# Kernel optimization log

Measured on AMD Instinct MI355X. Metric: run time of the kernel, lower is better.

Reference implementation:

```python
import jax, jax.numpy as jnp
import numpy as np

N_NODES = 100000
N_EDGES = 1600000
DIM = 64
BN_EPS = 1e-5


def setup_inputs() -> dict:
    key = jax.random.key(0)
    ks = jax.random.split(key, 6)
    x = jax.random.normal(ks[0], (N_NODES, DIM), dtype=jnp.float32)
    edge_index = jax.random.randint(ks[1], (2, N_EDGES), 0, N_NODES, dtype=jnp.int32)
    W = jax.random.normal(ks[2], (DIM, DIM), dtype=jnp.float32) / np.sqrt(DIM)
    b = jax.random.normal(ks[3], (DIM,), dtype=jnp.float32) * 0.01
    gamma = jnp.ones((DIM,), dtype=jnp.float32)
    beta = jnp.zeros((DIM,), dtype=jnp.float32)
    return {"x": x, "edge_index": edge_index, "W": W, "b": b, "gamma": gamma, "beta": beta}


def reference(x, edge_index, W, b, gamma, beta):
    n = x.shape[0]
    src, dst = edge_index[0], edge_index[1]
    # GCNConv adds self loops
    loop = jnp.arange(n, dtype=edge_index.dtype)
    src = jnp.concatenate([src, loop])
    dst = jnp.concatenate([dst, loop])
    # symmetric degree normalization: D^-1/2 (A+I) D^-1/2
    deg = jax.ops.segment_sum(jnp.ones(src.shape[0], x.dtype), dst, num_segments=n)
    dinv = jnp.where(deg > 0, jax.lax.rsqrt(deg), 0.0)
    norm = dinv[src] * dinv[dst]  # [E+N]
    h = x @ W  # [N, D] transform before aggregation (GCN order)
    msg = h[src] * norm[:, None]  # gather + scale
    out = jax.ops.segment_sum(msg, dst, num_segments=n) + b  # scatter-add
    # BatchNorm1d (training mode: batch statistics, biased variance)
    mean = jnp.mean(out, axis=0)
    var = jnp.mean(jnp.square(out - mean), axis=0)
    out = (out - mean) * jax.lax.rsqrt(var + BN_EPS) * gamma + beta
    # ReLU; dropout is identity in eval mode
    return jax.nn.relu(out)
```

## Files before the change

### kernel.cpp

```cpp
#include <hip/hip_runtime.h>

#define N_NODES 100000
#define N_EDGES 1600000
#define DIM 64
#define BN_EPS 1e-5f

#define BNODES 128
#define NBUCK ((N_NODES + BNODES - 1) / BNODES)
#define CAP_RAW 2560
#define CAP_OUT 3584
#define TILE 4096
#define ABLK ((N_EDGES + TILE - 1) / TILE)

#define GBLK 6250

typedef __bf16 bf16x8 __attribute__((ext_vector_type(8)));
typedef float floatx4 __attribute__((ext_vector_type(4)));

static __device__ __forceinline__ unsigned short f2bf(float f) {
    unsigned u = __float_as_uint(f);
    u = (u + 0x7FFFu + ((u >> 16) & 1u)) >> 16;
    return (unsigned short)u;
}
static __device__ __forceinline__ float bf2f(unsigned short h) {
    return __uint_as_float(((unsigned)h) << 16);
}

__global__ void __launch_bounds__(1024)
passA_kernel(const int* __restrict__ src, const int* __restrict__ dst,
             int* __restrict__ cur, unsigned int* __restrict__ entries, int E) {
    __shared__ int hist[NBUCK];
    __shared__ int lbase[NBUCK];
    int t = threadIdx.x;
    if (t < NBUCK) hist[t] = 0;
    __syncthreads();

    int e0   = blockIdx.x * TILE;
    int eend = min(e0 + TILE, E);

    int dreg[4], sreg[4], ne = 0;
    for (int e = e0 + t; e < eend; e += 1024) {
        dreg[ne] = dst[e];
        sreg[ne] = src[e];
        atomicAdd(&hist[dreg[ne] >> 7], 1);
        ++ne;
    }
    __syncthreads();
    if (t < NBUCK) {
        int ii = t + (blockIdx.x * 331) % NBUCK;
        if (ii >= NBUCK) ii -= NBUCK;
        int c = hist[ii];
        lbase[ii] = (c > 0) ? atomicAdd(&cur[ii], c) : 0;
        hist[ii] = 0;
    }
    __syncthreads();
    for (int k = 0; k < ne; ++k) {
        int s = sreg[k];
        int d = dreg[k];
        int b = d >> 7;
        int r = atomicAdd(&hist[b], 1);
        int pos = lbase[b] + r;
        if (pos < CAP_RAW)
            entries[(size_t)b * CAP_OUT + pos] = ((unsigned)s << 7) | (unsigned)(d & 127);
    }
}

__global__ void __launch_bounds__(256)
build_kernel(unsigned int* __restrict__ entries, const int* __restrict__ cur,
             int* __restrict__ rowbeg, int* __restrict__ rowend,
             float* __restrict__ dinv,
             const float* __restrict__ x, const float* __restrict__ W,
             unsigned short* __restrict__ hb, int dummyIdx, int N) {
    __shared__ unsigned int raw[CAP_RAW];
    __shared__ int hist[BNODES];
    __shared__ int sbuf[BNODES];
    __shared__ int startx[BNODES];
    __shared__ int cursor[BNODES];
    __shared__ float sdinv[BNODES];
    int bucket = blockIdx.x;
    int t = threadIdx.x;
    int node0 = bucket * BNODES;
    int nn = min(BNODES, N - node0);
    int cnt = min(cur[bucket], CAP_RAW);
    unsigned int* eb = entries + (size_t)bucket * CAP_OUT;

    if (t < BNODES) hist[t] = 0;
    __syncthreads();
    for (int i = t; i < cnt; i += 256) {
        unsigned int e = eb[i];
        raw[i] = e;
        atomicAdd(&hist[e & 127], 1);
    }
    __syncthreads();
    int pdeg_t = 0;
    if (t < BNODES) { pdeg_t = (hist[t] + 7) & ~7; sbuf[t] = pdeg_t; }
    __syncthreads();
    for (int off = 1; off < BNODES; off <<= 1) {
        int add = (t < BNODES && t >= off) ? sbuf[t - off] : 0;
        __syncthreads();
        if (t < BNODES) sbuf[t] += add;
        __syncthreads();
    }
    if (t < BNODES) {
        int ex = sbuf[t] - pdeg_t;
        startx[t] = ex;
        cursor[t] = ex;
    }
    __syncthreads();
    for (int i = t; i < cnt; i += 256) {
        unsigned int e = raw[i];
        int d = e & 127;
        int p = atomicAdd(&cursor[d], 1);
        eb[p] = e >> 7;
    }
    if (t < nn) {
        int dg  = hist[t];
        int pdg = (dg + 7) & ~7;
        int base = startx[t];
        for (int k = dg; k < pdg; ++k) eb[base + k] = (unsigned)dummyIdx;
        int gbase = bucket * CAP_OUT + base;
        rowbeg[node0 + t] = gbase;
        rowend[node0 + t] = gbase + pdg;
        float di = rsqrtf((float)(dg + 1));
        dinv[node0 + t] = di;
        sdinv[t] = di;
    }
    __syncthreads();

    int lane = t & 63, wv = t >> 6;
    int m = lane & 15, quad = lane >> 4;
    int nchunk = nn >> 4;
    if (wv < nchunk || nchunk == 8) {
        bf16x8 bfrag[2][4];
#pragma unroll
        for (int c = 0; c < 2; ++c)
#pragma unroll
            for (int nt = 0; nt < 4; ++nt) {
                bf16x8 f;
#pragma unroll
                for (int j = 0; j < 8; ++j) {
                    int k = c * 32 + quad * 8 + j;
                    f[j] = (__bf16)W[k * DIM + nt * 16 + m];
                }
                bfrag[c][nt] = f;
            }
        for (int c2 = wv; c2 < nchunk; c2 += 4) {
            int lrow0 = c2 * 16;
            int row0 = node0 + lrow0;
            const float* xr = x + (size_t)(row0 + m) * DIM;
            bf16x8 afrag[2];
#pragma unroll
            for (int c = 0; c < 2; ++c) {
                float4 lo = *(const float4*)(xr + c * 32 + quad * 8);
                float4 hi = *(const float4*)(xr + c * 32 + quad * 8 + 4);
                bf16x8 f;
                f[0] = (__bf16)lo.x; f[1] = (__bf16)lo.y; f[2] = (__bf16)lo.z; f[3] = (__bf16)lo.w;
                f[4] = (__bf16)hi.x; f[5] = (__bf16)hi.y; f[6] = (__bf16)hi.z; f[7] = (__bf16)hi.w;
                afrag[c] = f;
            }
            float dv[4];
#pragma unroll
            for (int r = 0; r < 4; ++r) dv[r] = sdinv[lrow0 + quad * 4 + r];
#pragma unroll
            for (int nt = 0; nt < 4; ++nt) {
                floatx4 acc = {0.f, 0.f, 0.f, 0.f};
                acc = __builtin_amdgcn_mfma_f32_16x16x32_bf16(afrag[0], bfrag[0][nt], acc, 0, 0, 0);
                acc = __builtin_amdgcn_mfma_f32_16x16x32_bf16(afrag[1], bfrag[1][nt], acc, 0, 0, 0);
#pragma unroll
                for (int r = 0; r < 4; ++r) {
                    int row = row0 + quad * 4 + r;
                    hb[(size_t)row * DIM + nt * 16 + m] = f2bf(acc[r] * dv[r]);
                }
            }
        }
    }
}

__global__ void __launch_bounds__(256)
gather_kernel(const int* __restrict__ rowbeg, const int* __restrict__ rowend,
              const unsigned int* __restrict__ srt, const unsigned short* __restrict__ hb,
              const float* __restrict__ dinv, float* __restrict__ out,
              float* __restrict__ partial, int N) {
    __shared__ float red[2][4][64];
    int lane = threadIdx.x & 63;
    int wv   = threadIdx.x >> 6;
    int g    = blockIdx.x * 4 + wv;
    int n0   = g << 2;
    float s_sum = 0.f, s_sq = 0.f;

    if (n0 < N) {
        int beg = __builtin_amdgcn_readfirstlane(rowbeg[n0]);
        int s1  = __builtin_amdgcn_readfirstlane(rowbeg[n0 + 1]);
        int s2  = __builtin_amdgcn_readfirstlane(rowbeg[n0 + 2]);
        int s3  = __builtin_amdgcn_readfirstlane(rowbeg[n0 + 3]);
        int end = __builtin_amdgcn_readfirstlane(rowend[n0 + 3]);
        float acc0 = 0.f, acc1 = 0.f, acc2 = 0.f, acc3 = 0.f;

        for (int base = beg; base < end; base += 64) {
            int idx = base + lane;
            unsigned int sv = (idx < end) ? srt[idx] : 0u;
            int cn = min(64, end - base);
            for (int j = 0; j < cn; j += 8) {
                int p0 = base + j;
                int k = (p0 >= s1) + (p0 >= s2) + (p0 >= s3);
                float v[8];
#pragma unroll
                for (int u = 0; u < 8; ++u) {
                    unsigned int s = (unsigned)__shfl((int)sv, j + u, 64);
                    v[u] = bf2f(hb[(size_t)s * DIM + lane]);
                }
                float csum = ((v[0] + v[1]) + (v[2] + v[3])) +
                             ((v[4] + v[5]) + (v[6] + v[7]));
                acc0 += (k == 0) ? csum : 0.f;
                acc1 += (k == 1) ? csum : 0.f;
                acc2 += (k == 2) ? csum : 0.f;
                acc3 += (k == 3) ? csum : 0.f;
            }
        }

        float v0 = (acc0 + bf2f(hb[(size_t)(n0 + 0) * DIM + lane])) * dinv[n0 + 0];
        float v1 = (acc1 + bf2f(hb[(size_t)(n0 + 1) * DIM + lane])) * dinv[n0 + 1];
        float v2 = (acc2 + bf2f(hb[(size_t)(n0 + 2) * DIM + lane])) * dinv[n0 + 2];
        float v3 = (acc3 + bf2f(hb[(size_t)(n0 + 3) * DIM + lane])) * dinv[n0 + 3];
        out[(size_t)(n0 + 0) * DIM + lane] = v0;
        out[(size_t)(n0 + 1) * DIM + lane] = v1;
        out[(size_t)(n0 + 2) * DIM + lane] = v2;
        out[(size_t)(n0 + 3) * DIM + lane] = v3;
        s_sum = ((v0 + v1) + (v2 + v3));
        s_sq  = ((v0 * v0 + v1 * v1) + (v2 * v2 + v3 * v3));
    }

    red[0][wv][lane] = s_sum;
    red[1][wv][lane] = s_sq;
    __syncthreads();
    if (threadIdx.x < 64) {
        int c = threadIdx.x;
        partial[(size_t)blockIdx.x * 128 + c] =
            red[0][0][c] + red[0][1][c] + red[0][2][c] + red[0][3][c];
        partial[(size_t)blockIdx.x * 128 + 64 + c] =
            red[1][0][c] + red[1][1][c] + red[1][2][c] + red[1][3][c];
    }
}

__global__ void reduce2_kernel(const float* __restrict__ partial, float* __restrict__ gstat) {
    __shared__ float buf[256];
    int t = threadIdx.x;
    int col = t & 127;
    int half = t >> 7;
    int r0 = blockIdx.x * 125;
    float acc = 0.f;
    for (int r = r0 + half; r < r0 + 125; r += 2)
        acc += partial[(size_t)r * 128 + col];
    buf[t] = acc;
    __syncthreads();
    if (t < 128) atomicAdd(&gstat[t], buf[t] + buf[t + 128]);
}

__global__ void __launch_bounds__(256)
finish_kernel(float4* __restrict__ out, const float* __restrict__ gstat,
              const float* __restrict__ gamma, const float* __restrict__ beta,
              int total4, int N) {
    __shared__ float scale[64];
    __shared__ float shift[64];
    int t = threadIdx.x;
    if (t < 64) {
        float invN = 1.0f / (float)N;
        float mean = gstat[t] * invN;
        float var  = gstat[64 + t] * invN - mean * mean;
        float sc   = gamma[t] * rsqrtf(var + BN_EPS);
        scale[t] = sc;
        shift[t] = beta[t] - mean * sc;
    }
    __syncthreads();
    int i = blockIdx.x * blockDim.x + t;
    if (i >= total4) return;
    int c = (i * 4) & 63;
    float4 v = out[i];
    float a0 = fmaf(v.x, scale[c],     shift[c]);
    float a1 = fmaf(v.y, scale[c + 1], shift[c + 1]);
    float a2 = fmaf(v.z, scale[c + 2], shift[c + 2]);
    float a3 = fmaf(v.w, scale[c + 3], shift[c + 3]);
    v.x = a0 > 0.f ? a0 : 0.f;
    v.y = a1 > 0.f ? a1 : 0.f;
    v.z = a2 > 0.f ? a2 : 0.f;
    v.w = a3 > 0.f ? a3 : 0.f;
    out[i] = v;
}

extern "C" void kernel_launch(void* const* d_in, const int* in_sizes, int n_in,
                              void* d_out, int out_size, void* d_ws, size_t ws_size,
                              hipStream_t stream) {
    const float* x     = (const float*)d_in[0];
    const int*   eidx  = (const int*)d_in[1];
    const float* W     = (const float*)d_in[2];
    const float* gamma = (const float*)d_in[4];
    const float* beta  = (const float*)d_in[5];
    float* out = (float*)d_out;

    const int N = N_NODES;
    const int total = N * DIM;

    const int* src = eidx;
    const int* dst = eidx + N_EDGES;

    char* ws = (char*)d_ws;
    size_t off_hb      = 0;
    size_t off_dinv    = off_hb + (size_t)N * DIM * 2;
    size_t off_rowbeg  = off_dinv + (size_t)N * 4;
    size_t off_rowend  = off_rowbeg + (size_t)N * 4;
    size_t off_entries = off_rowend + (size_t)N * 4;
    size_t off_partial = off_entries + (size_t)NBUCK * CAP_OUT * 4;
    size_t off_z       = off_partial + (size_t)GBLK * 128 * 4;

    unsigned short* hb    = (unsigned short*)(ws + off_hb);
    float*          dinv  = (float*)(ws + off_dinv);
    int*            rowbeg = (int*)(ws + off_rowbeg);
    int*            rowend = (int*)(ws + off_rowend);
    unsigned int*   entries = (unsigned int*)(ws + off_entries);
    float*          partial = (float*)(ws + off_partial);
    int*   cur   = (int*)(ws + off_z + 128);
    float* gstat = (float*)(cur + NBUCK);
    int dummyIdx = (int)(off_z / (DIM * 2));

    size_t zbytes = 128 + (size_t)NBUCK * 4 + 512;
    hipMemsetAsync(ws + off_z, 0, zbytes, stream);

    passA_kernel<<<ABLK, 1024, 0, stream>>>(src, dst, cur, entries, N_EDGES);

    build_kernel<<<NBUCK, 256, 0, stream>>>(entries, cur, rowbeg, rowend, dinv,
                                            x, W, hb, dummyIdx, N);

    gather_kernel<<<GBLK, 256, 0, stream>>>(rowbeg, rowend, entries, hb, dinv, out, partial, N);

    reduce2_kernel<<<50, 256, 0, stream>>>(partial, gstat);

    finish_kernel<<<(total / 4 + 255) / 256, 256, 0, stream>>>((float4*)out, gstat,
                                                               gamma, beta, total / 4, N);
}
```

Measured before the change: 197.7 us.

## Vectorize edge loads, sub-sort neighbors by source range, transpose MFMA stores, use readlane

```diff
diff --git a/kernel.cpp b/kernel.cpp
--- a/kernel.cpp
+++ b/kernel.cpp
@@ -37,14 +37,24 @@
 
     int e0   = blockIdx.x * TILE;
     int eend = min(e0 + TILE, E);
+    int eb   = e0 + t * 4;
 
     int dreg[4], sreg[4], ne = 0;
-    for (int e = e0 + t; e < eend; e += 1024) {
-        dreg[ne] = dst[e];
-        sreg[ne] = src[e];
-        atomicAdd(&hist[dreg[ne] >> 7], 1);
-        ++ne;
-    }
+    if (eb + 3 < eend) {
+        int4 d4 = *(const int4*)(dst + eb);
+        int4 s4 = *(const int4*)(src + eb);
+        dreg[0] = d4.x; dreg[1] = d4.y; dreg[2] = d4.z; dreg[3] = d4.w;
+        sreg[0] = s4.x; sreg[1] = s4.y; sreg[2] = s4.z; sreg[3] = s4.w;
+        ne = 4;
+    } else {
+        for (int e = eb; e < eend && ne < 4; ++e, ++ne) {
+            dreg[ne] = dst[e];
+            sreg[ne] = src[e];
+        }
+    }
+#pragma unroll
+    for (int k = 0; k < 4; ++k)
+        if (k < ne) atomicAdd(&hist[dreg[k] >> 7], 1);
     __syncthreads();
     if (t < NBUCK) {
         int ii = t + (blockIdx.x * 331) % NBUCK;
@@ -54,7 +64,9 @@
         hist[ii] = 0;
     }
     __syncthreads();
-    for (int k = 0; k < ne; ++k) {
+#pragma unroll
+    for (int k = 0; k < 4; ++k) {
+        if (k >= ne) break;
         int s = sreg[k];
         int d = dreg[k];
         int b = d >> 7;
@@ -72,10 +84,10 @@
              const float* __restrict__ x, const float* __restrict__ W,
              unsigned short* __restrict__ hb, int dummyIdx, int N) {
     __shared__ unsigned int raw[CAP_RAW];
-    __shared__ int hist[BNODES];
+    __shared__ int hist[BNODES * 4];
     __shared__ int sbuf[BNODES];
-    __shared__ int startx[BNODES];
-    __shared__ int cursor[BNODES];
+    __shared__ int nstart[BNODES];
+    __shared__ int cursor[BNODES * 4];
     __shared__ float sdinv[BNODES];
     int bucket = blockIdx.x;
     int t = threadIdx.x;
@@ -84,16 +96,22 @@
     int cnt = min(cur[bucket], CAP_RAW);
     unsigned int* eb = entries + (size_t)bucket * CAP_OUT;
 
-    if (t < BNODES) hist[t] = 0;
+    for (int i = t; i < BNODES * 4; i += 256) hist[i] = 0;
     __syncthreads();
     for (int i = t; i < cnt; i += 256) {
         unsigned int e = eb[i];
         raw[i] = e;
-        atomicAdd(&hist[e & 127], 1);
-    }
-    __syncthreads();
-    int pdeg_t = 0;
-    if (t < BNODES) { pdeg_t = (hist[t] + 7) & ~7; sbuf[t] = pdeg_t; }
+        int s = (int)(e >> 7);
+        int q = (s >= 25000) + (s >= 50000) + (s >= 75000);
+        atomicAdd(&hist[((e & 127) << 2) | q], 1);
+    }
+    __syncthreads();
+    int deg_t = 0, pdeg_t = 0;
+    if (t < BNODES) {
+        deg_t = hist[t * 4] + hist[t * 4 + 1] + hist[t * 4 + 2] + hist[t * 4 + 3];
+        pdeg_t = (deg_t + 7) & ~7;
+        sbuf[t] = pdeg_t;
+    }
     __syncthreads();
     for (int off = 1; off < BNODES; off <<= 1) {
         int add = (t < BNODES && t >= off) ? sbuf[t - off] : 0;
@@ -103,20 +121,25 @@
     }
     if (t < BNODES) {
         int ex = sbuf[t] - pdeg_t;
-        startx[t] = ex;
-        cursor[t] = ex;
+        nstart[t] = ex;
+        int o = ex;
+        cursor[t * 4 + 0] = o; o += hist[t * 4 + 0];
+        cursor[t * 4 + 1] = o; o += hist[t * 4 + 1];
+        cursor[t * 4 + 2] = o; o += hist[t * 4 + 2];
+        cursor[t * 4 + 3] = o;
     }
     __syncthreads();
     for (int i = t; i < cnt; i += 256) {
         unsigned int e = raw[i];
-        int d = e & 127;
-        int p = atomicAdd(&cursor[d], 1);
-        eb[p] = e >> 7;
+        int s = (int)(e >> 7);
+        int q = (s >= 25000) + (s >= 50000) + (s >= 75000);
+        int p = atomicAdd(&cursor[((e & 127) << 2) | q], 1);
+        eb[p] = (unsigned)s;
     }
     if (t < nn) {
-        int dg  = hist[t];
-        int pdg = (dg + 7) & ~7;
-        int base = startx[t];
+        int dg  = deg_t;
+        int pdg = pdeg_t;
+        int base = nstart[t];
         for (int k = dg; k < pdg; ++k) eb[base + k] = (unsigned)dummyIdx;
         int gbase = bucket * CAP_OUT + base;
         rowbeg[node0 + t] = gbase;
@@ -130,48 +153,45 @@
     int lane = t & 63, wv = t >> 6;
     int m = lane & 15, quad = lane >> 4;
     int nchunk = nn >> 4;
-    if (wv < nchunk || nchunk == 8) {
-        bf16x8 bfrag[2][4];
-#pragma unroll
-        for (int c = 0; c < 2; ++c)
-#pragma unroll
-            for (int nt = 0; nt < 4; ++nt) {
-                bf16x8 f;
-#pragma unroll
-                for (int j = 0; j < 8; ++j) {
-                    int k = c * 32 + quad * 8 + j;
-                    f[j] = (__bf16)W[k * DIM + nt * 16 + m];
-                }
-                bfrag[c][nt] = f;
+    bf16x8 bfrag[2][4];
+#pragma unroll
+    for (int c = 0; c < 2; ++c)
+#pragma unroll
+        for (int nt = 0; nt < 4; ++nt) {
+            bf16x8 f;
+#pragma unroll
+            for (int j = 0; j < 8; ++j) {
+                int k = c * 32 + quad * 8 + j;
+                f[j] = (__bf16)W[k * DIM + nt * 16 + m];
             }
-        for (int c2 = wv; c2 < nchunk; c2 += 4) {
-            int lrow0 = c2 * 16;
-            int row0 = node0 + lrow0;
-            const float* xr = x + (size_t)(row0 + m) * DIM;
-            bf16x8 afrag[2];
-#pragma unroll
-            for (int c = 0; c < 2; ++c) {
-                float4 lo = *(const float4*)(xr + c * 32 + quad * 8);
-                float4 hi = *(const float4*)(xr + c * 32 + quad * 8 + 4);
-                bf16x8 f;
-                f[0] = (__bf16)lo.x; f[1] = (__bf16)lo.y; f[2] = (__bf16)lo.z; f[3] = (__bf16)lo.w;
-                f[4] = (__bf16)hi.x; f[5] = (__bf16)hi.y; f[6] = (__bf16)hi.z; f[7] = (__bf16)hi.w;
-                afrag[c] = f;
-            }
-            float dv[4];
-#pragma unroll
-            for (int r = 0; r < 4; ++r) dv[r] = sdinv[lrow0 + quad * 4 + r];
-#pragma unroll
-            for (int nt = 0; nt < 4; ++nt) {
-                floatx4 acc = {0.f, 0.f, 0.f, 0.f};
-                acc = __builtin_amdgcn_mfma_f32_16x16x32_bf16(afrag[0], bfrag[0][nt], acc, 0, 0, 0);
-                acc = __builtin_amdgcn_mfma_f32_16x16x32_bf16(afrag[1], bfrag[1][nt], acc, 0, 0, 0);
-#pragma unroll
-                for (int r = 0; r < 4; ++r) {
-                    int row = row0 + quad * 4 + r;
-                    hb[(size_t)row * DIM + nt * 16 + m] = f2bf(acc[r] * dv[r]);
-                }
-            }
+            bfrag[c][nt] = f;
+        }
+    for (int c2 = wv; c2 < nchunk; c2 += 4) {
+        int lrow0 = c2 * 16;
+        int row0 = node0 + lrow0;
+        const float* xr = x + (size_t)(row0 + m) * DIM;
+        bf16x8 afrag[2];
+#pragma unroll
+        for (int c = 0; c < 2; ++c) {
+            float4 lo = *(const float4*)(xr + c * 32 + quad * 8);
+            float4 hi = *(const float4*)(xr + c * 32 + quad * 8 + 4);
+            bf16x8 f;
+            f[0] = (__bf16)lo.x; f[1] = (__bf16)lo.y; f[2] = (__bf16)lo.z; f[3] = (__bf16)lo.w;
+            f[4] = (__bf16)hi.x; f[5] = (__bf16)hi.y; f[6] = (__bf16)hi.z; f[7] = (__bf16)hi.w;
+            afrag[c] = f;
+        }
+        float dv = sdinv[lrow0 + m];
+#pragma unroll
+        for (int nt = 0; nt < 4; ++nt) {
+            floatx4 acc = {0.f, 0.f, 0.f, 0.f};
+            acc = __builtin_amdgcn_mfma_f32_16x16x32_bf16(bfrag[0][nt], afrag[0], acc, 0, 0, 0);
+            acc = __builtin_amdgcn_mfma_f32_16x16x32_bf16(bfrag[1][nt], afrag[1], acc, 0, 0, 0);
+            ushort4 pk;
+            pk.x = f2bf(acc[0] * dv);
+            pk.y = f2bf(acc[1] * dv);
+            pk.z = f2bf(acc[2] * dv);
+            pk.w = f2bf(acc[3] * dv);
+            *(ushort4*)(hb + (size_t)(row0 + m) * DIM + nt * 16 + quad * 4) = pk;
         }
     }
 }
@@ -206,7 +226,7 @@
                 float v[8];
 #pragma unroll
                 for (int u = 0; u < 8; ++u) {
-                    unsigned int s = (unsigned)__shfl((int)sv, j + u, 64);
+                    unsigned int s = (unsigned)__builtin_amdgcn_readlane((int)sv, j + u);
                     v[u] = bf2f(hb[(size_t)s * DIM + lane]);
                 }
                 float csum = ((v[0] + v[1]) + (v[2] + v[3])) +
```

Result: no change. 194.1 us (-1.8%).
